# Performance work log

Measured on AMD Instinct MI355X. Metric: run time of the kernel, lower is better.

## Reference

```python
import jax, jax.numpy as jnp
import numpy as np

VOCAB = 50000
DIM = 300
BATCH = 1024
CTX = 10


def setup_inputs() -> dict:
    key = jax.random.key(0)
    k1, k2, k3, k4 = jax.random.split(key, 4)
    context = jax.random.randint(k1, (BATCH, CTX), 0, VOCAB, dtype=jnp.int64 if jax.config.read('jax_enable_x64') else jnp.int32)
    W_proj = jax.random.normal(k2, (DIM, VOCAB), dtype=jnp.float32) * 0.02
    W_cls = jax.random.normal(k3, (VOCAB, DIM), dtype=jnp.float32) * 0.02
    b_cls = jax.random.normal(k4, (VOCAB,), dtype=jnp.float32) * 0.02
    return {"context": context, "W_proj": W_proj, "W_cls": W_cls, "b_cls": b_cls, "pad_idx": 0}


def reference(context, W_proj, W_cls, b_cls, pad_idx):
    # One-hot @ W_proj.T == gather of W_proj columns at context ids: [B, C, D]
    emb = jnp.take(W_proj, context, axis=1)            # [D, B, C]
    emb = jnp.moveaxis(emb, 0, -1)                     # [B, C, D]
    # zeroing the pad_idx column of the one-hot kills pad tokens' contribution,
    # but the mean still divides by the full context length C.
    mask = (context != pad_idx).astype(emb.dtype)      # [B, C]
    emb = emb * mask[..., None]
    pooled = emb.mean(axis=1)                          # [B, D]
    logits = pooled @ W_cls.T + b_cls                  # [B, V]
    return jax.nn.log_softmax(logits, axis=1)
```

## Files before the change

kernel.cpp:

```cpp
#include <hip/hip_runtime.h>
#include <math.h>

#define B_SZ 1024
#define CTXL 10
#define DIM  300
#define VOC  50000
#define KP   320
#define BM   128
#define BN   128
#define BK   64
#define NTIL 391
#define NSG  50
#define WROW 1200
#define WMAXOFF 59999984

typedef short s16x8 __attribute__((ext_vector_type(8)));
typedef float f32x4 __attribute__((ext_vector_type(4)));

__device__ __forceinline__ void gload_lds16(const void* g, void* lds) {
  __builtin_amdgcn_global_load_lds((const __attribute__((address_space(1))) void*)g,
                                   (__attribute__((address_space(3))) void*)lds, 16, 0, 0);
}

__global__ void pool_kernel(const int* __restrict__ ctx, const float* __restrict__ Wproj,
                            const int* __restrict__ padp, __bf16* __restrict__ pooled) {
  const int b = blockIdx.x;
  const int d = threadIdx.x;
  const int pad = *padp;
  float s = 0.f;
  if (d < DIM) {
#pragma unroll
    for (int c = 0; c < CTXL; ++c) {
      int id = ctx[b * CTXL + c];
      if (id != pad) s += Wproj[d * VOC + id];
    }
  }
  pooled[b * KP + d] = (__bf16)(s * 0.1f);
}

__global__ __launch_bounds__(256, 3) void gemm_kernel(const __bf16* __restrict__ A,
                                                      const float* __restrict__ Wcls,
                                                      const float* __restrict__ bias,
                                                      float* __restrict__ out,
                                                      float* __restrict__ sumexp) {
  __shared__ __align__(16) char smem[49152];
  const int bid = blockIdx.x;
  const int s = bid & 7;
  const int mj = (bid >> 3) & 7;
  const int G = bid >> 6;
  const int nt = G * 8 + s;
  if (nt >= NTIL) return;
  const int m0 = mj * BM;
  const int n0 = nt * BN;
  const int t = threadIdx.x;
  const int lane = t & 63;
  const int wave = t >> 6;
  const int wm = wave >> 1, wn = wave & 1;

  f32x4 acc[4][4];
#pragma unroll
  for (int i = 0; i < 4; ++i)
#pragma unroll
    for (int j = 0; j < 4; ++j) acc[i][j] = (f32x4){0.f, 0.f, 0.f, 0.f};

  const char* Ab = (const char*)A;
  const char* Wb = (const char*)Wcls;
  const int hi = lane >> 4;

  for (int k0 = 0; k0 < KP; k0 += BK) {
    {
      const int lr = lane >> 3;
      const int gc = (lane & 7) ^ lr;
#pragma unroll
      for (int i = 0; i < 4; ++i) {
        const int r = wave * 32 + i * 8 + lr;
        gload_lds16(Ab + (m0 + r) * (KP * 2) + k0 * 2 + gc * 16,
                    smem + wave * 4096 + i * 1024);
      }
    }
    {
      const int lr = lane >> 4;
#pragma unroll
      for (int i = 0; i < 8; ++i) {
        const int r = wave * 32 + i * 4 + lr;
        const int gc = (lane & 15) ^ (r & 7);
        int rowg = n0 + r; if (rowg > VOC - 1) rowg = VOC - 1;
        int off = rowg * WROW + (k0 / 4 + gc) * 16;
        if (off > WMAXOFF) off = WMAXOFF;
        gload_lds16(Wb + off, smem + 16384 + wave * 8192 + i * 1024);
      }
    }
    __syncthreads();
#pragma unroll
    for (int kk = 0; kk < 2; ++kk) {
      s16x8 af[4], bfr[4];
#pragma unroll
      for (int mf = 0; mf < 4; ++mf) {
        const int ra = wm * 64 + mf * 16 + (lane & 15);
        af[mf] = *(const s16x8*)(smem + ra * 128 + (((kk * 4 + hi) ^ (ra & 7)) * 16));
      }
#pragma unroll
      for (int nf = 0; nf < 4; ++nf) {
        const int rb = wn * 64 + nf * 16 + (lane & 15);
        const int cb = kk * 8 + hi * 2;
        const f32x4 x0 = *(const f32x4*)(smem + 16384 + rb * 256 + ((cb ^ (rb & 7)) * 16));
        const f32x4 x1 = *(const f32x4*)(smem + 16384 + rb * 256 + (((cb + 1) ^ (rb & 7)) * 16));
        union { __bf16 h; short v; } cv;
        s16x8 bb;
        cv.h = (__bf16)x0[0]; bb[0] = cv.v;
        cv.h = (__bf16)x0[1]; bb[1] = cv.v;
        cv.h = (__bf16)x0[2]; bb[2] = cv.v;
        cv.h = (__bf16)x0[3]; bb[3] = cv.v;
        cv.h = (__bf16)x1[0]; bb[4] = cv.v;
        cv.h = (__bf16)x1[1]; bb[5] = cv.v;
        cv.h = (__bf16)x1[2]; bb[6] = cv.v;
        cv.h = (__bf16)x1[3]; bb[7] = cv.v;
        bfr[nf] = bb;
      }
#pragma unroll
      for (int mf = 0; mf < 4; ++mf)
#pragma unroll
        for (int nf = 0; nf < 4; ++nf)
          acc[mf][nf] = __builtin_amdgcn_mfma_f32_16x16x32_bf16(af[mf], bfr[nf], acc[mf][nf], 0, 0, 0);
    }
    __syncthreads();
  }

  const int cl = lane & 15, lg = lane >> 4;
#pragma unroll
  for (int mf = 0; mf < 4; ++mf) {
    float rs[4] = {0.f, 0.f, 0.f, 0.f};
#pragma unroll
    for (int nf = 0; nf < 4; ++nf) {
      const int col = n0 + wn * 64 + nf * 16 + cl;
      const bool valid = col < VOC;
      const float bia = valid ? bias[col] : -1e30f;
#pragma unroll
      for (int reg = 0; reg < 4; ++reg) {
        const int row = m0 + wm * 64 + mf * 16 + lg * 4 + reg;
        const float logit = acc[mf][nf][reg] + bia;
        if (valid) out[row * VOC + col] = logit;
        rs[reg] += expf(logit);
      }
    }
#pragma unroll
    for (int reg = 0; reg < 4; ++reg) {
      float v = rs[reg];
      v += __shfl_xor(v, 1, 16);
      v += __shfl_xor(v, 2, 16);
      v += __shfl_xor(v, 4, 16);
      v += __shfl_xor(v, 8, 16);
      if (cl == 0) {
        const int row = m0 + wm * 64 + mf * 16 + lg * 4 + reg;
        atomicAdd(&sumexp[row], v);
      }
    }
  }
}

__global__ void lse_kernel(const float* __restrict__ sumexp, float* __restrict__ lse) {
  const int b = blockIdx.x * blockDim.x + threadIdx.x;
  if (b < B_SZ) lse[b] = logf(sumexp[b]);
}

__global__ void finalize_kernel(float* __restrict__ out, const float* __restrict__ lse) {
  const int i = blockIdx.x * 256 + threadIdx.x;
  const int b = blockIdx.y;
  if (i < VOC / 4) {
    const float l = lse[b];
    float4* p = (float4*)out + b * (VOC / 4) + i;
    float4 v = *p;
    v.x -= l; v.y -= l; v.z -= l; v.w -= l;
    *p = v;
  }
}

extern "C" void kernel_launch(void* const* d_in, const int* in_sizes, int n_in,
                              void* d_out, int out_size, void* d_ws, size_t ws_size,
                              hipStream_t stream) {
  (void)in_sizes; (void)n_in; (void)out_size;
  const int*   ctx   = (const int*)d_in[0];
  const float* Wproj = (const float*)d_in[1];
  const float* Wcls  = (const float*)d_in[2];
  const float* bcls  = (const float*)d_in[3];
  const int*   padp  = (const int*)d_in[4];
  float* out = (float*)d_out;

  if (ws_size < 663552) return;
  char* ws = (char*)d_ws;
  __bf16* pooled = (__bf16*)ws;
  float*  sumexp = (float*)(ws + 655360);
  float*  lse    = (float*)(ws + 655360 + 4096);

  hipMemsetAsync(sumexp, 0, B_SZ * sizeof(float), stream);
  pool_kernel<<<B_SZ, KP, 0, stream>>>(ctx, Wproj, padp, pooled);
  gemm_kernel<<<NSG * 64, 256, 0, stream>>>(pooled, Wcls, bcls, out, sumexp);
  lse_kernel<<<4, 256, 0, stream>>>(sumexp, lse);
  finalize_kernel<<<dim3(49, B_SZ), 256, 0, stream>>>(out, lse);
}
```

Measured before the change: 497.7 us.

## Transpose W_proj for coalesced pooling and double-buffer GEMM with pre-converted bf16 B

Adds a tiled transpose of W_proj into the output buffer so the pooling gather reads contiguous rows instead of strided columns. The GEMM is restructured to double-buffer LDS, loading the next K tile of W_cls through registers and converting it to bf16 once before storing to LDS, which removes the per-fragment fp32-to-bf16 conversion and halves B smem reads. It also drops to 2 blocks per CU for the larger 64KB LDS and switches expf to __expf. The transpose adds a full 60MB read/write pass of W_proj, which may cost more than the uncoalesced gather it replaces.

```diff
diff --git a/kernel.cpp b/kernel.cpp
--- a/kernel.cpp
+++ b/kernel.cpp
@@ -22,7 +22,24 @@
                                    (__attribute__((address_space(3))) void*)lds, 16, 0, 0);
 }
 
-__global__ void pool_kernel(const int* __restrict__ ctx, const float* __restrict__ Wproj,
+__global__ void transpose_kernel(const float* __restrict__ W, float* __restrict__ WT) {
+  __shared__ float tile[32][33];
+  const int v0 = blockIdx.x * 32, d0 = blockIdx.y * 32;
+  const int tx = threadIdx.x & 31, ty = threadIdx.x >> 5;
+#pragma unroll
+  for (int i = 0; i < 32; i += 8) {
+    const int d = d0 + ty + i, v = v0 + tx;
+    tile[ty + i][tx] = (d < DIM && v < VOC) ? W[d * VOC + v] : 0.f;
+  }
+  __syncthreads();
+#pragma unroll
+  for (int i = 0; i < 32; i += 8) {
+    const int v = v0 + ty + i, d = d0 + tx;
+    if (v < VOC && d < DIM) WT[v * DIM + d] = tile[tx][ty + i];
+  }
+}
+
+__global__ void pool_kernel(const int* __restrict__ ctx, const float* __restrict__ WT,
                             const int* __restrict__ padp, __bf16* __restrict__ pooled) {
   const int b = blockIdx.x;
   const int d = threadIdx.x;
@@ -31,19 +48,19 @@
   if (d < DIM) {
 #pragma unroll
     for (int c = 0; c < CTXL; ++c) {
-      int id = ctx[b * CTXL + c];
-      if (id != pad) s += Wproj[d * VOC + id];
+      const int id = ctx[b * CTXL + c];
+      if (id != pad) s += WT[id * DIM + d];
     }
   }
   pooled[b * KP + d] = (__bf16)(s * 0.1f);
 }
 
-__global__ __launch_bounds__(256, 3) void gemm_kernel(const __bf16* __restrict__ A,
+__global__ __launch_bounds__(256, 2) void gemm_kernel(const __bf16* __restrict__ A,
                                                       const float* __restrict__ Wcls,
                                                       const float* __restrict__ bias,
                                                       float* __restrict__ out,
                                                       float* __restrict__ sumexp) {
-  __shared__ __align__(16) char smem[49152];
+  __shared__ __align__(16) char smem[65536];
   const int bid = blockIdx.x;
   const int s = bid & 7;
   const int mj = (bid >> 3) & 7;
@@ -66,62 +83,102 @@
   const char* Ab = (const char*)A;
   const char* Wb = (const char*)Wcls;
   const int hi = lane >> 4;
-
-  for (int k0 = 0; k0 < KP; k0 += BK) {
-    {
-      const int lr = lane >> 3;
-      const int gc = (lane & 7) ^ lr;
+  const int lr8 = lane >> 3;
+  const int gcA = (lane & 7) ^ lr8;
+  const int brow = t >> 1;
+  const int bhalf = t & 1;
+  int browg = n0 + brow; if (browg > VOC - 1) browg = VOC - 1;
+
+  {
+#pragma unroll
+    for (int i = 0; i < 4; ++i) {
+      const int r = wave * 32 + i * 8 + lr8;
+      gload_lds16(Ab + (m0 + r) * (KP * 2) + gcA * 16, smem + wave * 4096 + i * 1024);
+    }
+    f32x4 breg[8];
+#pragma unroll
+    for (int j = 0; j < 8; ++j) {
+      int off = browg * WROW + (bhalf * 8 + j) * 16;
+      if (off > WMAXOFF) off = WMAXOFF;
+      breg[j] = *(const f32x4*)(Wb + off);
+    }
+#pragma unroll
+    for (int jj = 0; jj < 4; ++jj) {
+      union { __bf16 h; short v; } cv;
+      s16x8 bb;
+      cv.h = (__bf16)breg[jj * 2][0];     bb[0] = cv.v;
+      cv.h = (__bf16)breg[jj * 2][1];     bb[1] = cv.v;
+      cv.h = (__bf16)breg[jj * 2][2];     bb[2] = cv.v;
+      cv.h = (__bf16)breg[jj * 2][3];     bb[3] = cv.v;
+      cv.h = (__bf16)breg[jj * 2 + 1][0]; bb[4] = cv.v;
+      cv.h = (__bf16)breg[jj * 2 + 1][1]; bb[5] = cv.v;
+      cv.h = (__bf16)breg[jj * 2 + 1][2]; bb[6] = cv.v;
+      cv.h = (__bf16)breg[jj * 2 + 1][3]; bb[7] = cv.v;
+      const int c = bhalf * 4 + jj;
+      *(s16x8*)(smem + 32768 + brow * 128 + ((c ^ (brow & 7)) * 16)) = bb;
+    }
+  }
+  __syncthreads();
+
+#pragma unroll
+  for (int k = 0; k < 5; ++k) {
+    char* bAc = smem + (k & 1) * 16384;
+    char* bBc = smem + 32768 + (k & 1) * 16384;
+    char* bAn = smem + ((k + 1) & 1) * 16384;
+    char* bBn = smem + 32768 + ((k + 1) & 1) * 16384;
+
+    f32x4 breg[8];
+    if (k < 4) {
+      const int k0n = (k + 1) * BK;
 #pragma unroll
       for (int i = 0; i < 4; ++i) {
-        const int r = wave * 32 + i * 8 + lr;
-        gload_lds16(Ab + (m0 + r) * (KP * 2) + k0 * 2 + gc * 16,
-                    smem + wave * 4096 + i * 1024);
-      }
-    }
-    {
-      const int lr = lane >> 4;
-#pragma unroll
-      for (int i = 0; i < 8; ++i) {
-        const int r = wave * 32 + i * 4 + lr;
-        const int gc = (lane & 15) ^ (r & 7);
-        int rowg = n0 + r; if (rowg > VOC - 1) rowg = VOC - 1;
-        int off = rowg * WROW + (k0 / 4 + gc) * 16;
+        const int r = wave * 32 + i * 8 + lr8;
+        gload_lds16(Ab + (m0 + r) * (KP * 2) + k0n * 2 + gcA * 16, bAn + wave * 4096 + i * 1024);
+      }
+#pragma unroll
+      for (int j = 0; j < 8; ++j) {
+        int off = browg * WROW + (k0n / 4 + bhalf * 8 + j) * 16;
         if (off > WMAXOFF) off = WMAXOFF;
-        gload_lds16(Wb + off, smem + 16384 + wave * 8192 + i * 1024);
-      }
-    }
-    __syncthreads();
+        breg[j] = *(const f32x4*)(Wb + off);
+      }
+    }
+
 #pragma unroll
     for (int kk = 0; kk < 2; ++kk) {
       s16x8 af[4], bfr[4];
 #pragma unroll
       for (int mf = 0; mf < 4; ++mf) {
         const int ra = wm * 64 + mf * 16 + (lane & 15);
-        af[mf] = *(const s16x8*)(smem + ra * 128 + (((kk * 4 + hi) ^ (ra & 7)) * 16));
+        af[mf] = *(const s16x8*)(bAc + ra * 128 + (((kk * 4 + hi) ^ (ra & 7)) * 16));
       }
 #pragma unroll
       for (int nf = 0; nf < 4; ++nf) {
         const int rb = wn * 64 + nf * 16 + (lane & 15);
-        const int cb = kk * 8 + hi * 2;
-        const f32x4 x0 = *(const f32x4*)(smem + 16384 + rb * 256 + ((cb ^ (rb & 7)) * 16));
-        const f32x4 x1 = *(const f32x4*)(smem + 16384 + rb * 256 + (((cb + 1) ^ (rb & 7)) * 16));
+        bfr[nf] = *(const s16x8*)(bBc + rb * 128 + (((kk * 4 + hi) ^ (rb & 7)) * 16));
+      }
+#pragma unroll
+      for (int mf = 0; mf < 4; ++mf)
+#pragma unroll
+        for (int nf = 0; nf < 4; ++nf)
+          acc[mf][nf] = __builtin_amdgcn_mfma_f32_16x16x32_bf16(af[mf], bfr[nf], acc[mf][nf], 0, 0, 0);
+    }
+
+    if (k < 4) {
+#pragma unroll
+      for (int jj = 0; jj < 4; ++jj) {
         union { __bf16 h; short v; } cv;
         s16x8 bb;
-        cv.h = (__bf16)x0[0]; bb[0] = cv.v;
-        cv.h = (__bf16)x0[1]; bb[1] = cv.v;
-        cv.h = (__bf16)x0[2]; bb[2] = cv.v;
-        cv.h = (__bf16)x0[3]; bb[3] = cv.v;
-        cv.h = (__bf16)x1[0]; bb[4] = cv.v;
-        cv.h = (__bf16)x1[1]; bb[5] = cv.v;
-        cv.h = (__bf16)x1[2]; bb[6] = cv.v;
-        cv.h = (__bf16)x1[3]; bb[7] = cv.v;
-        bfr[nf] = bb;
-      }
-#pragma unroll
-      for (int mf = 0; mf < 4; ++mf)
-#pragma unroll
-        for (int nf = 0; nf < 4; ++nf)
-          acc[mf][nf] = __builtin_amdgcn_mfma_f32_16x16x32_bf16(af[mf], bfr[nf], acc[mf][nf], 0, 0, 0);
+        cv.h = (__bf16)breg[jj * 2][0];     bb[0] = cv.v;
+        cv.h = (__bf16)breg[jj * 2][1];     bb[1] = cv.v;
+        cv.h = (__bf16)breg[jj * 2][2];     bb[2] = cv.v;
+        cv.h = (__bf16)breg[jj * 2][3];     bb[3] = cv.v;
+        cv.h = (__bf16)breg[jj * 2 + 1][0]; bb[4] = cv.v;
+        cv.h = (__bf16)breg[jj * 2 + 1][1]; bb[5] = cv.v;
+        cv.h = (__bf16)breg[jj * 2 + 1][2]; bb[6] = cv.v;
+        cv.h = (__bf16)breg[jj * 2 + 1][3]; bb[7] = cv.v;
+        const int c = bhalf * 4 + jj;
+        *(s16x8*)(bBn + brow * 128 + ((c ^ (brow & 7)) * 16)) = bb;
+      }
     }
     __syncthreads();
   }
@@ -140,7 +197,7 @@
         const int row = m0 + wm * 64 + mf * 16 + lg * 4 + reg;
         const float logit = acc[mf][nf][reg] + bia;
         if (valid) out[row * VOC + col] = logit;
-        rs[reg] += expf(logit);
+        rs[reg] += __expf(logit);
       }
     }
 #pragma unroll
@@ -191,9 +248,11 @@
   __bf16* pooled = (__bf16*)ws;
   float*  sumexp = (float*)(ws + 655360);
   float*  lse    = (float*)(ws + 655360 + 4096);
+  float*  WT     = out;
 
   hipMemsetAsync(sumexp, 0, B_SZ * sizeof(float), stream);
-  pool_kernel<<<B_SZ, KP, 0, stream>>>(ctx, Wproj, padp, pooled);
+  transpose_kernel<<<dim3(1563, 10), 256, 0, stream>>>(Wproj, WT);
+  pool_kernel<<<B_SZ, KP, 0, stream>>>(ctx, WT, padp, pooled);
   gemm_kernel<<<NSG * 64, 256, 0, stream>>>(pooled, Wcls, bcls, out, sumexp);
   lse_kernel<<<4, 256, 0, stream>>>(sumexp, lse);
   finalize_kernel<<<dim3(49, B_SZ), 256, 0, stream>>>(out, lse);
```

Result: slower. 526.0 us (+5.7%).
